# Performance work log

Hardware: AMD Instinct MI355X
Metric: run time of the kernel (lower is better)

## Reference

```python
import jax, jax.numpy as jnp
import numpy as np

EMBEDDING_DIM = 64
NUM_EMBEDDINGS = 512


def setup_inputs() -> dict:
    key = jax.random.key(0)
    k1, k2 = jax.random.split(key)
    inputs = jax.random.normal(k1, (64, 32, 32, EMBEDDING_DIM), dtype=jnp.float32)
    # codebook: (embedding_dim, num_embeddings), matching the Keras weight layout
    embeddings = jax.random.normal(k2, (EMBEDDING_DIM, NUM_EMBEDDINGS), dtype=jnp.float32)
    return {"inputs": inputs, "embeddings": embeddings}


def reference(inputs, embeddings):
    input_shape = inputs.shape
    flat = inputs.reshape(-1, EMBEDDING_DIM)  # [N, D]
    distances = (
        jnp.sum(flat * flat, axis=1, keepdims=True)
        + jnp.sum(embeddings * embeddings, axis=0, keepdims=True)
        - 2.0 * (flat @ embeddings)
    )  # [N, K]
    encoding_indices = jnp.argmin(distances, axis=1)  # [N]
    # one-hot @ embeddings.T == row gather from embeddings.T
    quantized = jnp.take(embeddings.T, encoding_indices, axis=0)  # [N, D]
    quantized = quantized.reshape(input_shape)
    return quantized, encoding_indices
```

## Files before the change

kernel.cpp:

```cpp
#include <hip/hip_runtime.h>

#define D 64
#define K 512
#define NT (K / 16)
#define TAU 0.01f

typedef float  f32x4  __attribute__((ext_vector_type(4)));
typedef short  bf16x8 __attribute__((ext_vector_type(8)));

__device__ inline unsigned short bf16_rne(float f) {
    union { float f; unsigned u; } v; v.f = f;
    unsigned r = v.u + 0x7FFFu + ((v.u >> 16) & 1u);
    return (unsigned short)(r >> 16);
}
__device__ inline float bf16_val(unsigned short b) {
    union { float f; unsigned u; } v; v.u = ((unsigned)b) << 16;
    return v.f;
}
__device__ inline void split8(const float* p, bf16x8& h, bf16x8& l) {
    float4 a = *(const float4*)p;
    float4 b = *(const float4*)(p + 4);
    float f[8] = {a.x, a.y, a.z, a.w, b.x, b.y, b.z, b.w};
#pragma unroll
    for (int j = 0; j < 8; ++j) {
        unsigned short hb = bf16_rne(f[j]);
        float lo = f[j] - bf16_val(hb);
        h[j] = (short)hb;
        l[j] = (short)bf16_rne(lo);
    }
}

__global__ void vq_prep(const float* __restrict__ emb,
                        float* __restrict__ embT,
                        float* __restrict__ enorm,
                        bf16x8* __restrict__ bhi,
                        bf16x8* __restrict__ blo) {
    int t = blockIdx.x * blockDim.x + threadIdx.x;
    int nt = t >> 7, c = (t >> 6) & 1, lane = t & 63;
    int k  = nt * 16 + (lane & 15);
    int d0 = c * 32 + ((lane >> 4) << 3);
    bf16x8 h, l;
#pragma unroll
    for (int j = 0; j < 8; ++j) {
        float xv = emb[(d0 + j) * K + k];
        unsigned short hb = bf16_rne(xv);
        float lo = xv - bf16_val(hb);
        h[j] = (short)hb;
        l[j] = (short)bf16_rne(lo);
    }
    int off = (nt * 2 + c) * 64 + lane;
    bhi[off] = h; blo[off] = l;

    if (t < K) {
        float s = 0.f;
#pragma unroll
        for (int d = 0; d < D; ++d) {
            float v = emb[d * K + t];
            embT[t * D + d] = v;
            s += v * v;
        }
        enorm[t] = s;
    }
}

__global__ __launch_bounds__(256, 2) void vq_mfma(
    const float* __restrict__ x,
    const float* __restrict__ embT,
    const float* __restrict__ enorm,
    const bf16x8* __restrict__ bhi,
    const bf16x8* __restrict__ blo,
    float* __restrict__ outq,
    float* __restrict__ outidx) {
    const int tid  = threadIdx.x;
    const int wave = __builtin_amdgcn_readfirstlane(tid >> 6);
    const int lane = tid & 63;
    const int col  = lane & 15;
    const int grp  = lane >> 4;
    const int rt0  = (blockIdx.x * 4 + wave) * 2;

    bf16x8 ah[2][2], al[2][2];
#pragma unroll
    for (int t = 0; t < 2; ++t) {
        const float* xr = x + (size_t)((rt0 + t) * 16 + col) * D + grp * 8;
        split8(xr,      ah[t][0], al[t][0]);
        split8(xr + 32, ah[t][1], al[t][1]);
    }

    float b1[2][4], b2[2][4];
    int   bi[2][4];
#pragma unroll
    for (int t = 0; t < 2; ++t)
#pragma unroll
        for (int q = 0; q < 4; ++q) {
            b1[t][q] = -3.4e38f; b2[t][q] = -3.4e38f; bi[t][q] = 0;
        }

#pragma unroll 2
    for (int nt = 0; nt < NT; ++nt) {
        int fo = (nt * 2) * 64 + lane;
        bf16x8 bh0 = bhi[fo], bh1 = bhi[fo + 64];
        bf16x8 bl0 = blo[fo], bl1 = blo[fo + 64];
        float env = enorm[nt * 16 + col] * -0.5f;
        f32x4 acc[2];
#pragma unroll
        for (int t = 0; t < 2; ++t) {
            acc[t] = f32x4{env, env, env, env};
            acc[t] = __builtin_amdgcn_mfma_f32_16x16x32_bf16(ah[t][0], bh0, acc[t], 0, 0, 0);
            acc[t] = __builtin_amdgcn_mfma_f32_16x16x32_bf16(ah[t][1], bh1, acc[t], 0, 0, 0);
            acc[t] = __builtin_amdgcn_mfma_f32_16x16x32_bf16(ah[t][0], bl0, acc[t], 0, 0, 0);
            acc[t] = __builtin_amdgcn_mfma_f32_16x16x32_bf16(ah[t][1], bl1, acc[t], 0, 0, 0);
            acc[t] = __builtin_amdgcn_mfma_f32_16x16x32_bf16(al[t][0], bh0, acc[t], 0, 0, 0);
            acc[t] = __builtin_amdgcn_mfma_f32_16x16x32_bf16(al[t][1], bh1, acc[t], 0, 0, 0);
        }
        int kk = nt * 16 + col;
#pragma unroll
        for (int t = 0; t < 2; ++t)
#pragma unroll
            for (int q = 0; q < 4; ++q) {
                float v = acc[t][q];
                bool gt = v > b1[t][q];
                b2[t][q] = gt ? b1[t][q] : fmaxf(b2[t][q], v);
                b1[t][q] = gt ? v : b1[t][q];
                bi[t][q] = gt ? kk : bi[t][q];
            }
    }

#pragma unroll
    for (int t = 0; t < 2; ++t)
#pragma unroll
        for (int q = 0; q < 4; ++q) {
            float v1 = b1[t][q], v2 = b2[t][q];
            int   i1 = bi[t][q];
#pragma unroll
            for (int m = 1; m <= 8; m <<= 1) {
                float o1 = __shfl_xor(v1, m);
                float o2 = __shfl_xor(v2, m);
                int   oi = __shfl_xor(i1, m);
                float nb2 = fmaxf(fminf(v1, o1), fmaxf(v2, o2));
                if (o1 > v1 || (o1 == v1 && oi < i1)) { v1 = o1; i1 = oi; }
                v2 = nb2;
            }
            b1[t][q] = v1; b2[t][q] = v2; bi[t][q] = i1;
        }

#pragma unroll
    for (int t = 0; t < 2; ++t)
#pragma unroll
        for (int q = 0; q < 4; ++q) {
            unsigned long long m = __ballot(b1[t][q] - b2[t][q] < TAU);
            if (m == 0ull) continue;
            for (int g = 0; g < 4; ++g) {
                if (!((m >> (g * 16)) & 1ull)) continue;
                int row = (rt0 + t) * 16 + g * 4 + q;
                const float4* x4 = (const float4*)(x + (size_t)row * D);
                float4 xr[16];
#pragma unroll
                for (int j = 0; j < 16; ++j) xr[j] = x4[j];
                float xn = 0.f;
#pragma unroll
                for (int j = 0; j < 16; ++j)
                    xn += xr[j].x * xr[j].x + xr[j].y * xr[j].y +
                          xr[j].z * xr[j].z + xr[j].w * xr[j].w;
                float best = 3.4e38f; int bb = 0;
#pragma unroll
                for (int kk = 0; kk < 8; ++kk) {
                    int k = lane * 8 + kk;
                    const float4* e4 = (const float4*)(embT + (size_t)k * D);
                    float d0 = 0.f, d1 = 0.f, d2 = 0.f, d3 = 0.f;
#pragma unroll
                    for (int j = 0; j < 4; ++j) {
                        float4 e0 = e4[j*4+0], e1 = e4[j*4+1];
                        float4 e2 = e4[j*4+2], e3 = e4[j*4+3];
                        d0 += xr[j*4+0].x*e0.x + xr[j*4+0].y*e0.y + xr[j*4+0].z*e0.z + xr[j*4+0].w*e0.w;
                        d1 += xr[j*4+1].x*e1.x + xr[j*4+1].y*e1.y + xr[j*4+1].z*e1.z + xr[j*4+1].w*e1.w;
                        d2 += xr[j*4+2].x*e2.x + xr[j*4+2].y*e2.y + xr[j*4+2].z*e2.z + xr[j*4+2].w*e2.w;
                        d3 += xr[j*4+3].x*e3.x + xr[j*4+3].y*e3.y + xr[j*4+3].z*e3.z + xr[j*4+3].w*e3.w;
                    }
                    float dist = (xn + enorm[k]) - 2.0f * ((d0 + d1) + (d2 + d3));
                    if (dist < best) { best = dist; bb = k; }
                }
#pragma unroll
                for (int mm = 1; mm <= 32; mm <<= 1) {
                    float od = __shfl_xor(best, mm);
                    int   oi = __shfl_xor(bb, mm);
                    if (od < best || (od == best && oi < bb)) { best = od; bb = oi; }
                }
                if (grp == g) bi[t][q] = bb;
            }
        }

#pragma unroll
    for (int t = 0; t < 2; ++t) {
        int rbase = (rt0 + t) * 16;
#pragma unroll
        for (int q = 0; q < 4; ++q) {
            if (col == q) {
                int row = rbase + grp * 4 + q;
                outidx[row] = (float)bi[t][q];
            }
        }
#pragma unroll
        for (int g = 0; g < 4; ++g)
#pragma unroll
            for (int q = 0; q < 4; ++q) {
                int kidx = __shfl(bi[t][q], g * 16);
                int row  = rbase + g * 4 + q;
                outq[(size_t)row * D + lane] = embT[(size_t)kidx * D + lane];
            }
    }
}

extern "C" void kernel_launch(void* const* d_in, const int* in_sizes, int n_in,
                              void* d_out, int out_size, void* d_ws, size_t ws_size,
                              hipStream_t stream) {
    const float* x   = (const float*)d_in[0];
    const float* emb = (const float*)d_in[1];
    int nrows = in_sizes[0] / D;

    char* w = (char*)d_ws;
    float*  embT   = (float*)w;   w += (size_t)K * D * 4;
    float*  enorm  = (float*)w;   w += (size_t)K * 4;
    bf16x8* bhi    = (bf16x8*)w;  w += (size_t)NT * 2 * 64 * 16;
    bf16x8* blo    = (bf16x8*)w;

    float* outq   = (float*)d_out;
    float* outidx = (float*)d_out + (size_t)nrows * D;

    vq_prep<<<16, 256, 0, stream>>>(emb, embT, enorm, bhi, blo);
    vq_mfma<<<nrows / 128, 256, 0, stream>>>(x, embT, enorm, bhi, blo,
                                             outq, outidx);
}
```

Before: 49.66 us.

## Software-pipeline codebook fragment loads and split MFMA chains into independent accumulators

Restructures the main distance loop to prefetch the next two codebook tiles (bf16 hi/lo fragments and norms) into registers while computing the current pair. The single serial six-MFMA accumulation chain per tile is split into three independent two-MFMA chains (hi*hi, hi*lo, lo*hi) that are summed afterwards, shortening dependency latency and exposing more MFMA parallelism. Costs more VGPRs, which may hurt occupancy under the 2-blocks launch bound, and changes the floating-point summation order slightly.

```diff
diff --git a/kernel.cpp b/kernel.cpp
--- a/kernel.cpp
+++ b/kernel.cpp
@@ -95,34 +95,61 @@
             b1[t][q] = -3.4e38f; b2[t][q] = -3.4e38f; bi[t][q] = 0;
         }
 
-#pragma unroll 2
-    for (int nt = 0; nt < NT; ++nt) {
-        int fo = (nt * 2) * 64 + lane;
-        bf16x8 bh0 = bhi[fo], bh1 = bhi[fo + 64];
-        bf16x8 bl0 = blo[fo], bl1 = blo[fo + 64];
-        float env = enorm[nt * 16 + col] * -0.5f;
-        f32x4 acc[2];
-#pragma unroll
-        for (int t = 0; t < 2; ++t) {
-            acc[t] = f32x4{env, env, env, env};
-            acc[t] = __builtin_amdgcn_mfma_f32_16x16x32_bf16(ah[t][0], bh0, acc[t], 0, 0, 0);
-            acc[t] = __builtin_amdgcn_mfma_f32_16x16x32_bf16(ah[t][1], bh1, acc[t], 0, 0, 0);
-            acc[t] = __builtin_amdgcn_mfma_f32_16x16x32_bf16(ah[t][0], bl0, acc[t], 0, 0, 0);
-            acc[t] = __builtin_amdgcn_mfma_f32_16x16x32_bf16(ah[t][1], bl1, acc[t], 0, 0, 0);
-            acc[t] = __builtin_amdgcn_mfma_f32_16x16x32_bf16(al[t][0], bh0, acc[t], 0, 0, 0);
-            acc[t] = __builtin_amdgcn_mfma_f32_16x16x32_bf16(al[t][1], bh1, acc[t], 0, 0, 0);
-        }
-        int kk = nt * 16 + col;
-#pragma unroll
-        for (int t = 0; t < 2; ++t)
-#pragma unroll
-            for (int q = 0; q < 4; ++q) {
-                float v = acc[t][q];
-                bool gt = v > b1[t][q];
-                b2[t][q] = gt ? b1[t][q] : fmaxf(b2[t][q], v);
-                b1[t][q] = gt ? v : b1[t][q];
-                bi[t][q] = gt ? kk : bi[t][q];
-            }
+    bf16x8 pf[2][4]; float pen[2];
+#pragma unroll
+    for (int u = 0; u < 2; ++u) {
+        int fo = u * 128 + lane;
+        pf[u][0] = bhi[fo]; pf[u][1] = bhi[fo + 64];
+        pf[u][2] = blo[fo]; pf[u][3] = blo[fo + 64];
+        pen[u] = enorm[u * 16 + col];
+    }
+
+    const f32x4 zero4 = {0.f, 0.f, 0.f, 0.f};
+    for (int it = 0; it < NT; it += 2) {
+        bf16x8 cb[2][4]; float cen[2];
+#pragma unroll
+        for (int u = 0; u < 2; ++u) {
+#pragma unroll
+            for (int j = 0; j < 4; ++j) cb[u][j] = pf[u][j];
+            cen[u] = pen[u];
+        }
+#pragma unroll
+        for (int u = 0; u < 2; ++u) {
+            int ntn = (it + 2 + u) & 31;
+            int fo = ntn * 128 + lane;
+            pf[u][0] = bhi[fo]; pf[u][1] = bhi[fo + 64];
+            pf[u][2] = blo[fo]; pf[u][3] = blo[fo + 64];
+            pen[u] = enorm[ntn * 16 + col];
+        }
+
+        f32x4 hh[2][2], hl[2][2], lh[2][2];
+#pragma unroll
+        for (int u = 0; u < 2; ++u)
+#pragma unroll
+            for (int t = 0; t < 2; ++t) {
+                hh[u][t] = __builtin_amdgcn_mfma_f32_16x16x32_bf16(ah[t][0], cb[u][0], zero4, 0, 0, 0);
+                hl[u][t] = __builtin_amdgcn_mfma_f32_16x16x32_bf16(ah[t][0], cb[u][2], zero4, 0, 0, 0);
+                lh[u][t] = __builtin_amdgcn_mfma_f32_16x16x32_bf16(al[t][0], cb[u][0], zero4, 0, 0, 0);
+                hh[u][t] = __builtin_amdgcn_mfma_f32_16x16x32_bf16(ah[t][1], cb[u][1], hh[u][t], 0, 0, 0);
+                hl[u][t] = __builtin_amdgcn_mfma_f32_16x16x32_bf16(ah[t][1], cb[u][3], hl[u][t], 0, 0, 0);
+                lh[u][t] = __builtin_amdgcn_mfma_f32_16x16x32_bf16(al[t][1], cb[u][1], lh[u][t], 0, 0, 0);
+            }
+
+#pragma unroll
+        for (int u = 0; u < 2; ++u) {
+            float env2 = cen[u] * -0.5f;
+            int kk = (it + u) * 16 + col;
+#pragma unroll
+            for (int t = 0; t < 2; ++t)
+#pragma unroll
+                for (int q = 0; q < 4; ++q) {
+                    float v = (hh[u][t][q] + hl[u][t][q]) + (lh[u][t][q] + env2);
+                    bool gt = v > b1[t][q];
+                    b2[t][q] = fmaxf(b2[t][q], fminf(b1[t][q], v));
+                    b1[t][q] = gt ? v : b1[t][q];
+                    bi[t][q] = gt ? kk : bi[t][q];
+                }
+        }
     }
 
 #pragma unroll
```

Result: slower. 58.81 us (+18.4%).
